# Performance work log

Measured on AMD Instinct MI355X. Metric: run time of the kernel, lower is better.

Reference implementation:

```python
import jax, jax.numpy as jnp
import numpy as np

EPS_NORM = 1e-8   # torch cosine_similarity norm eps
EPS_DEN = 1e-10
CLAMP_MAX = 1e10


def _cos_matrix(a, b):
    # rows of a vs rows of b: [Na, Nb] cosine similarity via normalized matmul
    an = a / jnp.clip(jnp.linalg.norm(a, axis=-1, keepdims=True), EPS_NORM)
    bn = b / jnp.clip(jnp.linalg.norm(b, axis=-1, keepdims=True), EPS_NORM)
    return an @ bn.T


def setup_inputs() -> dict:
    key = jax.random.key(0)
    k1, k2, k3, k4, k5 = jax.random.split(key, 5)
    N, D, M, C = 4096, 256, 2, 100
    return {
        "label_encodings": jax.random.normal(k1, (N, D), dtype=jnp.float32),
        "fusion_z": jax.random.normal(k2, (M, N, D), dtype=jnp.float32),
        "sample_embeddings": jax.random.normal(k3, (N, D), dtype=jnp.float32),
        "label_embeddings": jax.random.normal(k4, (N, D), dtype=jnp.float32),
        "labels": jax.random.randint(k5, (N,), 0, C, dtype=jnp.int64),
        "temperature": jnp.ones((), dtype=jnp.float32),
        "xi": jnp.ones((), dtype=jnp.float32),
    }


def reference(label_encodings, fusion_z, sample_embeddings, label_embeddings,
              labels, temperature, xi):
    # ---- class_prompt_contrastive_Learning ----
    sim = _cos_matrix(label_encodings, label_encodings)            # [N, N]
    e = jnp.minimum(jnp.exp(sim / temperature), CLAMP_MAX)
    mask = (labels[:, None] == labels[None, :])
    num = jnp.sum(e * mask, axis=1)
    den = jnp.clip(jnp.sum(e, axis=1), EPS_DEN)
    loss_class = jnp.mean(-jnp.log(num / den))

    # ---- supervised_cross_view_contrastive ----
    M, N, D = fusion_z.shape
    fz = fusion_z.reshape(M * N, D)
    lab_exp = jnp.tile(labels, M)                                  # labels.repeat(M)
    mask2 = (lab_exp[:, None] == lab_exp[None, :])
    sim2 = _cos_matrix(fz, fz)                                     # [MN, MN]
    e2 = jnp.exp(sim2 / temperature)
    num2 = jnp.sum(e2 * mask2, axis=1)
    den2 = jnp.clip(jnp.sum(e2, axis=1), EPS_DEN)
    loss_cross = jnp.mean(-jnp.log(num2 / den2))

    # ---- boundary_aware_independent_hashing ----
    cs = _cos_matrix(sample_embeddings, label_embeddings)          # [N, N]
    Dm = (1.0 - cs) * 0.5
    y = (labels[:, None] == labels[None, :]).astype(cs.dtype)
    loss_mat = y * Dm ** 2 + (1.0 - y) * jnp.maximum(xi - Dm, 0.0) ** 2
    loss_hash = jnp.mean(loss_mat)

    return jnp.stack([loss_class, loss_cross, loss_hash])
```

## Files before the change

kernel.cpp:

```cpp
#include <hip/hip_runtime.h>
#include <hip/hip_bf16.h>
#include <stdint.h>


typedef __attribute__((ext_vector_type(8))) short bf16x8;
typedef __attribute__((ext_vector_type(4))) float f32x4;

__device__ inline void gload_lds16(const void* g, void* l) {
  __builtin_amdgcn_global_load_lds(
      (__attribute__((address_space(1))) void*)g,
      (__attribute__((address_space(3))) void*)l, 16, 0, 0);
}

__device__ inline unsigned short f2bf(float x) {
  unsigned int u = __builtin_bit_cast(unsigned int, x);
  u = (u + 0x7fffu + ((u >> 16) & 1u)) >> 16;
  return (unsigned short)u;
}

__global__ __launch_bounds__(256) void norm_kernel(
    const float* __restrict__ LE, const float* __restrict__ FZ,
    const float* __restrict__ SE, const float* __restrict__ LM,
    unsigned short* __restrict__ An, unsigned short* __restrict__ Fn,
    unsigned short* __restrict__ Sn, unsigned short* __restrict__ Ln) {
  const int tid = threadIdx.x;
  const int wid = tid >> 6, lane = tid & 63;
  const int row = blockIdx.x * 4 + wid;

  const float* src;
  unsigned short* dst;
  int r;
  if (row < 4096)       { src = LE; dst = An; r = row; }
  else if (row < 12288) { src = FZ; dst = Fn; r = row - 4096; }
  else if (row < 16384) { src = SE; dst = Sn; r = row - 12288; }
  else                  { src = LM; dst = Ln; r = row - 16384; }

  const float4 v = *(const float4*)(src + (size_t)r * 256 + lane * 4);
  float ss = v.x * v.x + v.y * v.y + v.z * v.z + v.w * v.w;
#pragma unroll
  for (int m = 1; m < 64; m <<= 1) ss += __shfl_xor(ss, m);
  const float scale = 1.0f / fmaxf(sqrtf(ss), 1e-8f);

  ushort4 o;
  o.x = f2bf(v.x * scale);
  o.y = f2bf(v.y * scale);
  o.z = f2bf(v.z * scale);
  o.w = f2bf(v.w * scale);
  *(ushort4*)(dst + (size_t)r * 256 + lane * 4) = o;
}

__device__ inline void tri_decode(int t, int nb, int& rb, int& cb) {
  int r = 0;
  while (t >= nb - r) { t -= nb - r; ++r; }
  rb = r;
  cb = r + t;
}

__global__ __launch_bounds__(512) void fused_sim(
    const unsigned short* __restrict__ An, const unsigned short* __restrict__ Fn,
    const unsigned short* __restrict__ Sn, const unsigned short* __restrict__ Ln,
    const int* __restrict__ labels,
    const float* __restrict__ tp, const float* __restrict__ xip,
    float* __restrict__ numc, float* __restrict__ denc,
    float* __restrict__ numx, float* __restrict__ denx,
    float* __restrict__ hacc) {
  __shared__ __align__(16) char At[32768];
  __shared__ __align__(16) char Bt[32768];

  const int hw = blockIdx.x;
  const int bid = (hw & 7) * 115 + (hw >> 3);

  int mode, rb, cb;
  const unsigned short *X, *Y;
  float *nv = nullptr, *dv = nullptr;
  if (bid < 136) {
    mode = 0; tri_decode(bid, 16, rb, cb); X = An; Y = An; nv = numc; dv = denc;
  } else if (bid < 664) {
    mode = 1; tri_decode(bid - 136, 32, rb, cb); X = Fn; Y = Fn; nv = numx; dv = denx;
  } else {
    mode = 2; const int t = bid - 664; rb = t >> 4; cb = t & 15; X = Sn; Y = Ln;
  }

  const int tid = threadIdx.x;
  const int lane = tid & 63, wid = tid >> 6;
  const int wr = wid >> 2, wc = wid & 3;
  const int g = lane >> 4, c = lane & 15;

  f32x4 acc[8][4];
  const f32x4 zero = {0.f, 0.f, 0.f, 0.f};
#pragma unroll
  for (int m = 0; m < 8; ++m)
#pragma unroll
    for (int n = 0; n < 4; ++n) acc[m][n] = zero;

  const int srow = tid >> 3;
  const int sgl = ((tid >> 1) & 7) ^ (srow & 7);
  const char* xsrc = (const char*)X + ((size_t)rb * 256 + srow) * 512 + sgl * 16;
  const char* ysrc = (const char*)Y + ((size_t)cb * 256 + srow) * 512 + sgl * 16;
  char* ldsa = At + wid * 1024;
  char* ldsb = Bt + wid * 1024;

  const int pxs = c & 7;
  const char* aBase = At + (wr * 128 + c) * 128;
  const char* bBase = Bt + (wc * 64 + c) * 128;

  for (int kk = 0; kk < 4; ++kk) {
#pragma unroll
    for (int t = 0; t < 4; ++t) {
      gload_lds16(xsrc + (size_t)t * 32768 + kk * 128, ldsa + t * 8192);
      gload_lds16(ysrc + (size_t)t * 32768 + kk * 128, ldsb + t * 8192);
    }
    __syncthreads();
#pragma unroll
    for (int ks = 0; ks < 2; ++ks) {
      const int px = ((ks * 4 + g) ^ pxs) * 16;
      bf16x8 af[8], bg[4];
#pragma unroll
      for (int m = 0; m < 8; ++m) af[m] = *(const bf16x8*)(aBase + m * 2048 + px);
#pragma unroll
      for (int n = 0; n < 4; ++n) bg[n] = *(const bf16x8*)(bBase + n * 2048 + px);
#pragma unroll
      for (int m = 0; m < 8; ++m)
#pragma unroll
        for (int n = 0; n < 4; ++n)
          acc[m][n] = __builtin_amdgcn_mfma_f32_16x16x32_bf16(
              af[m], bg[n], acc[m][n], 0, 0, 0);
    }
    __syncthreads();
  }

  if (mode < 2) {
    const float invt = 1.0f / tp[0];
    const bool docol = (rb != cb);
    int collab[4];
#pragma unroll
    for (int n = 0; n < 4; ++n)
      collab[n] = labels[(cb * 256 + wc * 64 + n * 16 + c) & 4095];

    float* sc = (float*)At;
    sc[tid] = 0.f;
    sc[tid + 512] = 0.f;
    __syncthreads();
    float* rowN = sc, *rowD = sc + 256, *colN = sc + 512, *colD = sc + 768;

    float cn[4] = {0.f, 0.f, 0.f, 0.f}, cd[4] = {0.f, 0.f, 0.f, 0.f};
#pragma unroll
    for (int m = 0; m < 8; ++m) {
#pragma unroll
      for (int reg = 0; reg < 4; ++reg) {
        const int rloc = wr * 128 + m * 16 + g * 4 + reg;
        const int rlab = labels[(rb * 256 + rloc) & 4095];
        float pn = 0.f, pd = 0.f;
#pragma unroll
        for (int n = 0; n < 4; ++n) {
          float e = __expf(acc[m][n][reg] * invt);
          if (mode == 0) e = fminf(e, 1e10f);
          pd += e;
          const bool eq = (rlab == collab[n]);
          const float en = eq ? e : 0.f;
          pn += en;
          if (docol) { cd[n] += e; cn[n] += en; }
        }
#pragma unroll
        for (int msk = 1; msk < 16; msk <<= 1) {
          pn += __shfl_xor(pn, msk);
          pd += __shfl_xor(pd, msk);
        }
        if (c == 0) {
          atomicAdd(&rowN[rloc], pn);
          atomicAdd(&rowD[rloc], pd);
        }
      }
    }
    if (docol) {
#pragma unroll
      for (int n = 0; n < 4; ++n) {
        float a = cn[n], b = cd[n];
        a += __shfl_xor(a, 16); b += __shfl_xor(b, 16);
        a += __shfl_xor(a, 32); b += __shfl_xor(b, 32);
        if (g == 0) {
          const int cl = wc * 64 + n * 16 + c;
          atomicAdd(&colN[cl], a);
          atomicAdd(&colD[cl], b);
        }
      }
    }
    __syncthreads();
    if (tid < 256) {
      atomicAdd(&nv[rb * 256 + tid], rowN[tid]);
      atomicAdd(&dv[rb * 256 + tid], rowD[tid]);
    } else if (docol) {
      atomicAdd(&nv[cb * 256 + (tid - 256)], colN[tid - 256]);
      atomicAdd(&dv[cb * 256 + (tid - 256)], colD[tid - 256]);
    }
  } else {
    const float xi = xip[0];
    int collab[4];
#pragma unroll
    for (int n = 0; n < 4; ++n)
      collab[n] = labels[(cb * 256 + wc * 64 + n * 16 + c) & 4095];
    float part = 0.f;
#pragma unroll
    for (int m = 0; m < 8; ++m)
#pragma unroll
      for (int reg = 0; reg < 4; ++reg) {
        const int rlab = labels[(rb * 256 + wr * 128 + m * 16 + g * 4 + reg) & 4095];
#pragma unroll
        for (int n = 0; n < 4; ++n) {
          const float cs = acc[m][n][reg];
          const float Dm = (1.0f - cs) * 0.5f;
          const float u = fmaxf(xi - Dm, 0.0f);
          part += (rlab == collab[n]) ? Dm * Dm : u * u;
        }
      }
#pragma unroll
    for (int msk = 1; msk < 64; msk <<= 1) part += __shfl_xor(part, msk);
    float* hp = (float*)At;
    if (lane == 0) hp[wid] = part;
    __syncthreads();
    if (tid == 0) {
      float s = 0.f;
#pragma unroll
      for (int w = 0; w < 8; ++w) s += hp[w];
      atomicAdd(hacc, s);
    }
  }
}

__global__ __launch_bounds__(256) void finalize_kernel(
    const float* __restrict__ numc, const float* __restrict__ denc,
    const float* __restrict__ numx, const float* __restrict__ denx,
    const float* __restrict__ hacc, float* __restrict__ out) {
  const int tid = threadIdx.x;
  float s1 = 0.f, s2 = 0.f;
  for (int i = tid; i < 4096; i += 256)
    s1 += -logf(numc[i] / fmaxf(denc[i], 1e-10f));
  for (int i = tid; i < 8192; i += 256)
    s2 += -logf(numx[i] / fmaxf(denx[i], 1e-10f));
#pragma unroll
  for (int m = 1; m < 64; m <<= 1) {
    s1 += __shfl_xor(s1, m);
    s2 += __shfl_xor(s2, m);
  }
  __shared__ float r1[4], r2[4];
  const int wid = tid >> 6;
  if ((tid & 63) == 0) { r1[wid] = s1; r2[wid] = s2; }
  __syncthreads();
  if (tid == 0) {
    out[0] = (r1[0] + r1[1] + r1[2] + r1[3]) / 4096.0f;
    out[1] = (r2[0] + r2[1] + r2[2] + r2[3]) / 8192.0f;
    out[2] = hacc[0] / (4096.0f * 4096.0f);
  }
}

extern "C" void kernel_launch(void* const* d_in, const int* in_sizes, int n_in,
                              void* d_out, int out_size, void* d_ws,
                              size_t ws_size, hipStream_t stream) {
  const float* LE = (const float*)d_in[0];
  const float* FZ = (const float*)d_in[1];
  const float* SE = (const float*)d_in[2];
  const float* LM = (const float*)d_in[3];
  const int* labels = (const int*)d_in[4];
  const float* tp = (const float*)d_in[5];
  const float* xip = (const float*)d_in[6];
  float* out = (float*)d_out;

  char* ws = (char*)d_ws;
  unsigned short* An = (unsigned short*)(ws);
  unsigned short* Fn = (unsigned short*)(ws + 2097152);
  unsigned short* Sn = (unsigned short*)(ws + 6291456);
  unsigned short* Ln = (unsigned short*)(ws + 8388608);
  float* numc = (float*)(ws + 10485760);
  float* denc = numc + 4096;
  float* numx = denc + 4096;
  float* denx = numx + 8192;
  float* hacc = denx + 8192;

  hipMemsetAsync(numc, 0, (size_t)(4096 * 2 + 8192 * 2 + 1) * sizeof(float),
                 stream);

  norm_kernel<<<dim3(20480 / 4), dim3(256), 0, stream>>>(LE, FZ, SE, LM, An,
                                                         Fn, Sn, Ln);
  fused_sim<<<dim3(920), dim3(512), 0, stream>>>(An, Fn, Sn, Ln, labels, tp,
                                                 xip, numc, denc, numx, denx,
                                                 hacc);
  finalize_kernel<<<dim3(1), dim3(256), 0, stream>>>(numc, denc, numx, denx,
                                                     hacc, out);
}
```

Measured before the change: 195.9 us.

## Shrink similarity tiles to 128x128 with 256 threads, fold memset into norm kernel

Changes the fused similarity kernel from 256x256 tiles with 512 threads to 128x128 tiles with 256 threads and launch bounds allowing three blocks per CU. The grid grows from 920 to 3632 blocks, with halved LDS per block. The goals are higher occupancy and finer load balance across CUs. Label lookups are staged in shared memory, and LDS atomics in the epilogue become plain stores followed by a two-way sum. The zeroing memset is folded into the norm kernel and finalize is split across three blocks. In exchange, operands are reloaded more often because smaller tiles reuse data less, and more global atomics are issued.

```diff
diff --git a/kernel.cpp b/kernel.cpp
--- a/kernel.cpp
+++ b/kernel.cpp
@@ -22,8 +22,12 @@
     const float* __restrict__ LE, const float* __restrict__ FZ,
     const float* __restrict__ SE, const float* __restrict__ LM,
     unsigned short* __restrict__ An, unsigned short* __restrict__ Fn,
-    unsigned short* __restrict__ Sn, unsigned short* __restrict__ Ln) {
+    unsigned short* __restrict__ Sn, unsigned short* __restrict__ Ln,
+    float* __restrict__ zbuf) {
   const int tid = threadIdx.x;
+  const int zidx = blockIdx.x * 256 + tid;
+  if (zidx < 24577) zbuf[zidx] = 0.f;
+
   const int wid = tid >> 6, lane = tid & 63;
   const int row = blockIdx.x * 4 + wid;
 
@@ -56,7 +60,7 @@
   cb = r + t;
 }
 
-__global__ __launch_bounds__(512) void fused_sim(
+__global__ __launch_bounds__(256, 3) void fused_sim(
     const unsigned short* __restrict__ An, const unsigned short* __restrict__ Fn,
     const unsigned short* __restrict__ Sn, const unsigned short* __restrict__ Ln,
     const int* __restrict__ labels,
@@ -64,63 +68,71 @@
     float* __restrict__ numc, float* __restrict__ denc,
     float* __restrict__ numx, float* __restrict__ denx,
     float* __restrict__ hacc) {
-  __shared__ __align__(16) char At[32768];
-  __shared__ __align__(16) char Bt[32768];
+  __shared__ __align__(16) char At[16384];
+  __shared__ __align__(16) char Bt[16384];
+  __shared__ int lrS[128], lcS[128];
 
   const int hw = blockIdx.x;
-  const int bid = (hw & 7) * 115 + (hw >> 3);
+  const int bid = (hw & 7) * 454 + (hw >> 3);
 
   int mode, rb, cb;
   const unsigned short *X, *Y;
   float *nv = nullptr, *dv = nullptr;
-  if (bid < 136) {
-    mode = 0; tri_decode(bid, 16, rb, cb); X = An; Y = An; nv = numc; dv = denc;
-  } else if (bid < 664) {
-    mode = 1; tri_decode(bid - 136, 32, rb, cb); X = Fn; Y = Fn; nv = numx; dv = denx;
+  if (bid < 528) {
+    mode = 0; tri_decode(bid, 32, rb, cb); X = An; Y = An; nv = numc; dv = denc;
+  } else if (bid < 2608) {
+    mode = 1; tri_decode(bid - 528, 64, rb, cb); X = Fn; Y = Fn;
+    nv = numx; dv = denx;
   } else {
-    mode = 2; const int t = bid - 664; rb = t >> 4; cb = t & 15; X = Sn; Y = Ln;
+    mode = 2; const int t = bid - 2608; rb = t >> 5; cb = t & 31;
+    X = Sn; Y = Ln;
   }
 
   const int tid = threadIdx.x;
   const int lane = tid & 63, wid = tid >> 6;
-  const int wr = wid >> 2, wc = wid & 3;
+  const int wr = wid >> 1, wc = wid & 1;
   const int g = lane >> 4, c = lane & 15;
 
-  f32x4 acc[8][4];
+  if (tid < 128) lrS[tid] = labels[(rb * 128 + tid) & 4095];
+  else           lcS[tid - 128] = labels[(cb * 128 + (tid - 128)) & 4095];
+
+  f32x4 acc[4][4];
   const f32x4 zero = {0.f, 0.f, 0.f, 0.f};
 #pragma unroll
-  for (int m = 0; m < 8; ++m)
+  for (int m = 0; m < 4; ++m)
 #pragma unroll
     for (int n = 0; n < 4; ++n) acc[m][n] = zero;
 
   const int srow = tid >> 3;
-  const int sgl = ((tid >> 1) & 7) ^ (srow & 7);
-  const char* xsrc = (const char*)X + ((size_t)rb * 256 + srow) * 512 + sgl * 16;
-  const char* ysrc = (const char*)Y + ((size_t)cb * 256 + srow) * 512 + sgl * 16;
+  const int sgl = (tid & 7) ^ (srow & 7);
+  const char* xsrc =
+      (const char*)X + ((size_t)rb * 128 + srow) * 512 + sgl * 16;
+  const char* ysrc =
+      (const char*)Y + ((size_t)cb * 128 + srow) * 512 + sgl * 16;
   char* ldsa = At + wid * 1024;
   char* ldsb = Bt + wid * 1024;
 
+  const char* aBase = At + (wr * 64 + c) * 128;
+  const char* bBase = Bt + (wc * 64 + c) * 128;
   const int pxs = c & 7;
-  const char* aBase = At + (wr * 128 + c) * 128;
-  const char* bBase = Bt + (wc * 64 + c) * 128;
 
   for (int kk = 0; kk < 4; ++kk) {
 #pragma unroll
     for (int t = 0; t < 4; ++t) {
-      gload_lds16(xsrc + (size_t)t * 32768 + kk * 128, ldsa + t * 8192);
-      gload_lds16(ysrc + (size_t)t * 32768 + kk * 128, ldsb + t * 8192);
+      gload_lds16(xsrc + (size_t)t * 16384 + kk * 128, ldsa + t * 4096);
+      gload_lds16(ysrc + (size_t)t * 16384 + kk * 128, ldsb + t * 4096);
     }
     __syncthreads();
 #pragma unroll
     for (int ks = 0; ks < 2; ++ks) {
       const int px = ((ks * 4 + g) ^ pxs) * 16;
-      bf16x8 af[8], bg[4];
-#pragma unroll
-      for (int m = 0; m < 8; ++m) af[m] = *(const bf16x8*)(aBase + m * 2048 + px);
+      bf16x8 af[4], bg[4];
+#pragma unroll
+      for (int m = 0; m < 4; ++m) af[m] = *(const bf16x8*)(aBase + m * 2048 + px);
 #pragma unroll
       for (int n = 0; n < 4; ++n) bg[n] = *(const bf16x8*)(bBase + n * 2048 + px);
 #pragma unroll
-      for (int m = 0; m < 8; ++m)
+      for (int m = 0; m < 4; ++m)
 #pragma unroll
         for (int n = 0; n < 4; ++n)
           acc[m][n] = __builtin_amdgcn_mfma_f32_16x16x32_bf16(
@@ -134,22 +146,19 @@
     const bool docol = (rb != cb);
     int collab[4];
 #pragma unroll
-    for (int n = 0; n < 4; ++n)
-      collab[n] = labels[(cb * 256 + wc * 64 + n * 16 + c) & 4095];
+    for (int n = 0; n < 4; ++n) collab[n] = lcS[wc * 64 + n * 16 + c];
 
     float* sc = (float*)At;
-    sc[tid] = 0.f;
-    sc[tid + 512] = 0.f;
-    __syncthreads();
     float* rowN = sc, *rowD = sc + 256, *colN = sc + 512, *colD = sc + 768;
 
     float cn[4] = {0.f, 0.f, 0.f, 0.f}, cd[4] = {0.f, 0.f, 0.f, 0.f};
-#pragma unroll
-    for (int m = 0; m < 8; ++m) {
+    float rn[16], rd[16];
+#pragma unroll
+    for (int m = 0; m < 4; ++m) {
 #pragma unroll
       for (int reg = 0; reg < 4; ++reg) {
-        const int rloc = wr * 128 + m * 16 + g * 4 + reg;
-        const int rlab = labels[(rb * 256 + rloc) & 4095];
+        const int rloc = wr * 64 + m * 16 + g * 4 + reg;
+        const int rlab = lrS[rloc];
         float pn = 0.f, pd = 0.f;
 #pragma unroll
         for (int n = 0; n < 4; ++n) {
@@ -159,52 +168,59 @@
           const bool eq = (rlab == collab[n]);
           const float en = eq ? e : 0.f;
           pn += en;
-          if (docol) { cd[n] += e; cn[n] += en; }
+          cd[n] += e;
+          cn[n] += en;
         }
 #pragma unroll
         for (int msk = 1; msk < 16; msk <<= 1) {
           pn += __shfl_xor(pn, msk);
           pd += __shfl_xor(pd, msk);
         }
+        rn[m * 4 + reg] = pn;
+        rd[m * 4 + reg] = pd;
+      }
+    }
+    __syncthreads();
+#pragma unroll
+    for (int m = 0; m < 4; ++m)
+#pragma unroll
+      for (int reg = 0; reg < 4; ++reg) {
+        const int rloc = wr * 64 + m * 16 + g * 4 + reg;
         if (c == 0) {
-          atomicAdd(&rowN[rloc], pn);
-          atomicAdd(&rowD[rloc], pd);
-        }
-      }
-    }
-    if (docol) {
-#pragma unroll
-      for (int n = 0; n < 4; ++n) {
-        float a = cn[n], b = cd[n];
-        a += __shfl_xor(a, 16); b += __shfl_xor(b, 16);
-        a += __shfl_xor(a, 32); b += __shfl_xor(b, 32);
-        if (g == 0) {
-          const int cl = wc * 64 + n * 16 + c;
-          atomicAdd(&colN[cl], a);
-          atomicAdd(&colD[cl], b);
-        }
-      }
-    }
-    __syncthreads();
-    if (tid < 256) {
-      atomicAdd(&nv[rb * 256 + tid], rowN[tid]);
-      atomicAdd(&dv[rb * 256 + tid], rowD[tid]);
+          rowN[wc * 128 + rloc] = rn[m * 4 + reg];
+          rowD[wc * 128 + rloc] = rd[m * 4 + reg];
+        }
+      }
+#pragma unroll
+    for (int n = 0; n < 4; ++n) {
+      float a = cn[n], b = cd[n];
+      a += __shfl_xor(a, 16); b += __shfl_xor(b, 16);
+      a += __shfl_xor(a, 32); b += __shfl_xor(b, 32);
+      if (g == 0) {
+        colN[wr * 128 + wc * 64 + n * 16 + c] = a;
+        colD[wr * 128 + wc * 64 + n * 16 + c] = b;
+      }
+    }
+    __syncthreads();
+    if (tid < 128) {
+      atomicAdd(&nv[rb * 128 + tid], rowN[tid] + rowN[128 + tid]);
+      atomicAdd(&dv[rb * 128 + tid], rowD[tid] + rowD[128 + tid]);
     } else if (docol) {
-      atomicAdd(&nv[cb * 256 + (tid - 256)], colN[tid - 256]);
-      atomicAdd(&dv[cb * 256 + (tid - 256)], colD[tid - 256]);
+      const int cl = tid - 128;
+      atomicAdd(&nv[cb * 128 + cl], colN[cl] + colN[128 + cl]);
+      atomicAdd(&dv[cb * 128 + cl], colD[cl] + colD[128 + cl]);
     }
   } else {
     const float xi = xip[0];
     int collab[4];
 #pragma unroll
-    for (int n = 0; n < 4; ++n)
-      collab[n] = labels[(cb * 256 + wc * 64 + n * 16 + c) & 4095];
+    for (int n = 0; n < 4; ++n) collab[n] = lcS[wc * 64 + n * 16 + c];
     float part = 0.f;
 #pragma unroll
-    for (int m = 0; m < 8; ++m)
+    for (int m = 0; m < 4; ++m)
 #pragma unroll
       for (int reg = 0; reg < 4; ++reg) {
-        const int rlab = labels[(rb * 256 + wr * 128 + m * 16 + g * 4 + reg) & 4095];
+        const int rlab = lrS[wr * 64 + m * 16 + g * 4 + reg];
 #pragma unroll
         for (int n = 0; n < 4; ++n) {
           const float cs = acc[m][n][reg];
@@ -216,14 +232,10 @@
 #pragma unroll
     for (int msk = 1; msk < 64; msk <<= 1) part += __shfl_xor(part, msk);
     float* hp = (float*)At;
+    __syncthreads();
     if (lane == 0) hp[wid] = part;
     __syncthreads();
-    if (tid == 0) {
-      float s = 0.f;
-#pragma unroll
-      for (int w = 0; w < 8; ++w) s += hp[w];
-      atomicAdd(hacc, s);
-    }
+    if (tid == 0) atomicAdd(hacc, hp[0] + hp[1] + hp[2] + hp[3]);
   }
 }
 
@@ -232,25 +244,23 @@
     const float* __restrict__ numx, const float* __restrict__ denx,
     const float* __restrict__ hacc, float* __restrict__ out) {
   const int tid = threadIdx.x;
-  float s1 = 0.f, s2 = 0.f;
-  for (int i = tid; i < 4096; i += 256)
-    s1 += -logf(numc[i] / fmaxf(denc[i], 1e-10f));
-  for (int i = tid; i < 8192; i += 256)
-    s2 += -logf(numx[i] / fmaxf(denx[i], 1e-10f));
-#pragma unroll
-  for (int m = 1; m < 64; m <<= 1) {
-    s1 += __shfl_xor(s1, m);
-    s2 += __shfl_xor(s2, m);
-  }
-  __shared__ float r1[4], r2[4];
-  const int wid = tid >> 6;
-  if ((tid & 63) == 0) { r1[wid] = s1; r2[wid] = s2; }
+  const int b = blockIdx.x;
+  if (b == 2) {
+    if (tid == 0) out[2] = hacc[0] / (4096.0f * 4096.0f);
+    return;
+  }
+  const float* num = (b == 0) ? numc : numx;
+  const float* den = (b == 0) ? denc : denx;
+  const int n = (b == 0) ? 4096 : 8192;
+  float s = 0.f;
+  for (int i = tid; i < n; i += 256)
+    s += -logf(num[i] / fmaxf(den[i], 1e-10f));
+#pragma unroll
+  for (int m = 1; m < 64; m <<= 1) s += __shfl_xor(s, m);
+  __shared__ float r[4];
+  if ((tid & 63) == 0) r[tid >> 6] = s;
   __syncthreads();
-  if (tid == 0) {
-    out[0] = (r1[0] + r1[1] + r1[2] + r1[3]) / 4096.0f;
-    out[1] = (r2[0] + r2[1] + r2[2] + r2[3]) / 8192.0f;
-    out[2] = hacc[0] / (4096.0f * 4096.0f);
-  }
+  if (tid == 0) out[b] = (r[0] + r[1] + r[2] + r[3]) / (float)n;
 }
 
 extern "C" void kernel_launch(void* const* d_in, const int* in_sizes, int n_in,
@@ -276,14 +286,11 @@
   float* denx = numx + 8192;
   float* hacc = denx + 8192;
 
-  hipMemsetAsync(numc, 0, (size_t)(4096 * 2 + 8192 * 2 + 1) * sizeof(float),
-                 stream);
-
-  norm_kernel<<<dim3(20480 / 4), dim3(256), 0, stream>>>(LE, FZ, SE, LM, An,
-                                                         Fn, Sn, Ln);
-  fused_sim<<<dim3(920), dim3(512), 0, stream>>>(An, Fn, Sn, Ln, labels, tp,
-                                                 xip, numc, denc, numx, denx,
-                                                 hacc);
-  finalize_kernel<<<dim3(1), dim3(256), 0, stream>>>(numc, denc, numx, denx,
+  norm_kernel<<<dim3(5120), dim3(256), 0, stream>>>(LE, FZ, SE, LM, An, Fn,
+                                                    Sn, Ln, numc);
+  fused_sim<<<dim3(3632), dim3(256), 0, stream>>>(An, Fn, Sn, Ln, labels, tp,
+                                                  xip, numc, denc, numx, denx,
+                                                  hacc);
+  finalize_kernel<<<dim3(3), dim3(256), 0, stream>>>(numc, denc, numx, denx,
                                                      hacc, out);
 }
```

Measured after the change: 175.8 us. 1.11x faster.
